# Performance work log

Measured on AMD Instinct MI355X. Metric: run time of the kernel, lower is better.

## Reference

```python
import jax, jax.numpy as jnp
import numpy as np

B, C, H, W = 8, 512, 32, 32
N_HEADS = 4
D_K = C // N_HEADS  # 128


def setup_inputs() -> dict:
    key = jax.random.key(0)
    k1, k2, k3, k4, k5 = jax.random.split(key, 5)
    x = jax.random.normal(k1, (B, C, H, W), dtype=jnp.float32)
    # projection: Linear(in_ch, n_heads*d_k*3)
    Wp = jax.random.normal(k2, (C, N_HEADS * D_K * 3), dtype=jnp.float32) * (C ** -0.5)
    bp = jax.random.normal(k3, (N_HEADS * D_K * 3,), dtype=jnp.float32) * 0.01
    # output: Linear(n_heads*d_k, in_ch)
    Wo = jax.random.normal(k4, (N_HEADS * D_K, C), dtype=jnp.float32) * ((N_HEADS * D_K) ** -0.5)
    bo = jax.random.normal(k5, (C,), dtype=jnp.float32) * 0.01
    return {"x": x, "Wp": Wp, "bp": bp, "Wo": Wo, "bo": bo}


def reference(x, Wp, bp, Wo, bo):
    b, c, h, w = x.shape
    scale = D_K ** -0.5
    # [B, C, H, W] -> [B, N, C], N = H*W
    xs = x.reshape(b, c, h * w).transpose(0, 2, 1)
    qkv = (xs @ Wp + bp).reshape(b, h * w, N_HEADS, 3 * D_K)
    q, k, v = jnp.split(qkv, 3, axis=-1)  # each [B, N, H, D]
    attn = jnp.einsum('bihd,bjhd->bijh', q, k) * scale
    attn = jax.nn.softmax(attn, axis=2)  # softmax over j (keys)
    out = jnp.einsum('bijh,bjhd->bihd', attn, v)
    out = out.reshape(b, h * w, N_HEADS * D_K)
    out = out @ Wo + bo
    out = out + xs  # residual (note: GroupNorm is unused in the original forward)
    return out.transpose(0, 2, 1).reshape(b, c, h, w)
```

## Files before the change

kernel.cpp:

```cpp
#include <hip/hip_runtime.h>

#define NB 8
#define NC 512
#define NTOK 1024
#define NHEADS 4
#define DKH 128

typedef unsigned short u16;
typedef __attribute__((ext_vector_type(8))) short bf16x8;
typedef __attribute__((ext_vector_type(4))) float f32x4;

__device__ inline u16 f2b(float f) {
    union { float f; unsigned u; } v; v.f = f;
    unsigned r = v.u + 0x7fffu + ((v.u >> 16) & 1u);
    return (u16)(r >> 16);
}

__device__ __forceinline__ void gll16(const u16* g, u16* l) {
    __builtin_amdgcn_global_load_lds((const __attribute__((address_space(1))) unsigned*)g,
                                     (__attribute__((address_space(3))) unsigned*)l, 16, 0, 0);
}

__global__ __launch_bounds__(256) void prep(const float* __restrict__ x, const float* __restrict__ Wp,
                                            const float* __restrict__ Wo,
                                            u16* __restrict__ xsb, u16* __restrict__ WpT, u16* __restrict__ WoT)
{
    __shared__ float tile[32][33];
    const int z = blockIdx.z;
    const float* src; u16* dst; int R, Cc;
    if (z == 0)      { src = Wp; dst = WpT; R = 512; Cc = 1536; }
    else if (z == 1) { if (blockIdx.x >= 16) return; src = Wo; dst = WoT; R = 512; Cc = 512; }
    else             { if (blockIdx.x >= 32) return;
                       src = x + (long)(z-2)*NC*NTOK; dst = xsb + (long)(z-2)*NTOK*NC; R = NC; Cc = NTOK; }
    int c0 = blockIdx.x * 32, r0 = blockIdx.y * 32;
    int tx = threadIdx.x, ty = threadIdx.y;
    #pragma unroll
    for (int k = 0; k < 4; ++k)
        tile[ty + 8*k][tx] = src[(long)(r0 + ty + 8*k) * Cc + c0 + tx];
    __syncthreads();
    #pragma unroll
    for (int k = 0; k < 4; ++k)
        dst[(long)(c0 + ty + 8*k) * R + r0 + tx] = f2b(tile[tx][ty + 8*k]);
}

__global__ __launch_bounds__(256) void gemm_qkv(const u16* __restrict__ WpT, const u16* __restrict__ xsb,
                                                const float* __restrict__ bp,
                                                u16* __restrict__ qg, u16* __restrict__ kg, u16* __restrict__ vg)
{
    __shared__ union SmU {
        struct { u16 As[128][64]; u16 Bs[128][64]; } s;
        u16 Os[4][64][72];
    } sm;
    const int tid = threadIdx.x;
    const int m0 = blockIdx.x * 128;
    const int n0 = blockIdx.y * 128;
    const int w = tid >> 6, lane = tid & 63, quad = lane >> 4, lc = lane & 15;
    const int mo = (w & 1) * 64, no = (w >> 1) * 64;
    const int sw8 = (((lane & 7) ^ (lane >> 3)) << 3);
    const int xs = lc & 7;

    f32x4 acc[4][4] = {};

    for (int k0 = 0; k0 < NC; k0 += 64) {
        __syncthreads();
        #pragma unroll
        for (int p = 0; p < 4; ++p) {
            int row = w*32 + p*8 + (lane >> 3);
            gll16(&WpT[(long)(m0 + row) * NC + k0 + sw8], &sm.s.As[w*32 + p*8][0]);
            gll16(&xsb[(long)(n0 + row) * NC + k0 + sw8], &sm.s.Bs[w*32 + p*8][0]);
        }
        __syncthreads();
        #pragma unroll
        for (int ks = 0; ks < 2; ++ks) {
            bf16x8 af[4], bfr[4];
            #pragma unroll
            for (int t = 0; t < 4; ++t) {
                af[t]  = *(const bf16x8*)&sm.s.As[mo + t*16 + lc][((ks*4 + quad) ^ xs) << 3];
                bfr[t] = *(const bf16x8*)&sm.s.Bs[no + t*16 + lc][((ks*4 + quad) ^ xs) << 3];
            }
            #pragma unroll
            for (int mt = 0; mt < 4; ++mt)
                #pragma unroll
                for (int nt = 0; nt < 4; ++nt)
                    acc[mt][nt] = __builtin_amdgcn_mfma_f32_16x16x32_bf16(af[mt], bfr[nt], acc[mt][nt], 0, 0, 0);
        }
    }
    __syncthreads();

    const int bb = n0 >> 10;
    const int nblk = n0 & 1023;
    const int cqb = m0 + mo;
    const int h = cqb / 384;
    const int rem = cqb - h * 384;
    const int sel = rem >> 7;
    const int d_base = rem & 127;

    #pragma unroll
    for (int mt = 0; mt < 4; ++mt) {
        int cq0 = cqb + mt*16 + quad*4;
        float b0 = bp[cq0+0], b1 = bp[cq0+1], b2 = bp[cq0+2], b3 = bp[cq0+3];
        #pragma unroll
        for (int nt = 0; nt < 4; ++nt) {
            f32x4 a = acc[mt][nt];
            int nl = nt*16 + lc;
            int ml = mt*16 + quad*4;
            u16 e0 = f2b(a[0]+b0), e1 = f2b(a[1]+b1), e2 = f2b(a[2]+b2), e3 = f2b(a[3]+b3);
            if (sel == 2) {
                sm.Os[w][ml+0][nl] = e0; sm.Os[w][ml+1][nl] = e1;
                sm.Os[w][ml+2][nl] = e2; sm.Os[w][ml+3][nl] = e3;
            } else {
                sm.Os[w][nl][ml+0] = e0; sm.Os[w][nl][ml+1] = e1;
                sm.Os[w][nl][ml+2] = e2; sm.Os[w][nl][ml+3] = e3;
            }
        }
    }
    __builtin_amdgcn_sched_barrier(0);

    const long bhbase = (long)(bb * NHEADS + h);
    const int sw = sw8;
    if (sel == 2) {
        #pragma unroll
        for (int pass = 0; pass < 8; ++pass) {
            int ml  = pass*8 + (lane >> 3);
            int nl0 = (lane & 7) * 8;
            bf16x8 vv = *(const bf16x8*)&sm.Os[w][ml][nl0];
            *(bf16x8*)&vg[((bhbase*DKH + d_base + ml) << 10) + nblk + no + sw] = vv;
        }
    } else if (sel == 1) {
        #pragma unroll
        for (int pass = 0; pass < 8; ++pass) {
            int nl  = pass*8 + (lane >> 3);
            int ml0 = (lane & 7) * 8;
            bf16x8 vv = *(const bf16x8*)&sm.Os[w][nl][ml0];
            *(bf16x8*)&kg[((bhbase*NTOK + nblk + no + nl) << 7) + d_base + sw] = vv;
        }
    } else {
        #pragma unroll
        for (int pass = 0; pass < 8; ++pass) {
            int nl  = pass*8 + (lane >> 3);
            int ml0 = (lane & 7) * 8;
            bf16x8 vv = *(const bf16x8*)&sm.Os[w][nl][ml0];
            *(bf16x8*)&qg[((bhbase*NTOK + nblk + no + nl) << 7) + d_base + ml0] = vv;
        }
    }
}

__global__ __launch_bounds__(256) void attn(const u16* __restrict__ qg, const u16* __restrict__ kg,
                                            const u16* __restrict__ vtg, u16* __restrict__ ho)
{
    __shared__ u16 Ks[2][64*128];
    __shared__ u16 Vt[2][128*64];
    __shared__ u16 Ps[4][32][72];
    const int tid = threadIdx.x;
    const int w = tid >> 6, lane = tid & 63, quad = lane >> 4, lc = lane & 15;
    const int id = blockIdx.x;
    const int xcd = id & 7, rest = id >> 3, sub = rest & 3, bx = rest >> 2;
    const int pr = xcd + sub*8;
    const int b = pr >> 2, h = pr & 3;
    const int i0 = bx*128 + w*32;
    const long bh = (long)(b * NHEADS + h) << 17;
    const u16* qb = qg + bh;
    const u16* kb = kg + bh;
    const u16* vb = vtg + bh;
    const float SL2E = 0.08838834764831845f * 1.4426950408889634f;

    bf16x8 qf[2][4];
    #pragma unroll
    for (int ib = 0; ib < 2; ++ib)
        #pragma unroll
        for (int ks = 0; ks < 4; ++ks)
            qf[ib][ks] = *(const bf16x8*)&qb[(long)(i0 + ib*16 + lc) * DKH + ks*32 + quad*8];

    f32x4 o[2][8] = {};
    float lsum[2] = {0.f, 0.f};
    const int xs = lc & 7;

    #pragma unroll
    for (int p = 0; p < 4; ++p) {
        int ck = (w*4 + p)*64 + lane;
        gll16(&kb[(long)ck * 8], &Ks[0][(w*4 + p)*512]);
        gll16(&vb[(((long)(ck >> 3)) << 10) + (ck & 7)*8], &Vt[0][(w*4 + p)*512]);
    }

    for (int t = 0; t < 16; ++t) {
        __syncthreads();
        if (t < 15) {
            long jo = (long)(t+1) * 64;
            #pragma unroll
            for (int p = 0; p < 4; ++p) {
                int ck = (w*4 + p)*64 + lane;
                gll16(&kb[jo*128 + (long)ck*8], &Ks[(t+1)&1][(w*4 + p)*512]);
                gll16(&vb[(((long)(ck >> 3)) << 10) + jo + (ck & 7)*8], &Vt[(t+1)&1][(w*4 + p)*512]);
            }
        }
        const u16* K = Ks[t&1];
        const u16* V = Vt[t&1];

        f32x4 s[2][4] = {};
        #pragma unroll
        for (int ks = 0; ks < 4; ++ks)
            #pragma unroll
            for (int jt = 0; jt < 4; ++jt) {
                bf16x8 kf = *(const bf16x8*)&K[(jt*16 + lc)*128 + (((ks*4 + quad) ^ xs) << 3)];
                s[0][jt] = __builtin_amdgcn_mfma_f32_16x16x32_bf16(kf, qf[0][ks], s[0][jt], 0, 0, 0);
                s[1][jt] = __builtin_amdgcn_mfma_f32_16x16x32_bf16(kf, qf[1][ks], s[1][jt], 0, 0, 0);
            }

        #pragma unroll
        for (int ib = 0; ib < 2; ++ib)
            #pragma unroll
            for (int jt = 0; jt < 4; ++jt) {
                float p0 = __builtin_amdgcn_exp2f(s[ib][jt][0] * SL2E);
                float p1 = __builtin_amdgcn_exp2f(s[ib][jt][1] * SL2E);
                float p2 = __builtin_amdgcn_exp2f(s[ib][jt][2] * SL2E);
                float p3 = __builtin_amdgcn_exp2f(s[ib][jt][3] * SL2E);
                lsum[ib] += (p0 + p1) + (p2 + p3);
                ushort4 pk;
                pk.x = f2b(p0); pk.y = f2b(p1); pk.z = f2b(p2); pk.w = f2b(p3);
                *(ushort4*)&Ps[w][ib*16 + lc][jt*16 + quad*4] = pk;
            }
        __builtin_amdgcn_sched_barrier(0);

        #pragma unroll
        for (int ks2 = 0; ks2 < 2; ++ks2) {
            bf16x8 pf0 = *(const bf16x8*)&Ps[w][lc][ks2*32 + quad*8];
            bf16x8 pf1 = *(const bf16x8*)&Ps[w][16 + lc][ks2*32 + quad*8];
            #pragma unroll
            for (int dt = 0; dt < 8; ++dt) {
                bf16x8 vf = *(const bf16x8*)&V[(dt*16 + lc)*64 + (((ks2*4 + quad) ^ xs) << 3)];
                o[0][dt] = __builtin_amdgcn_mfma_f32_16x16x32_bf16(vf, pf0, o[0][dt], 0, 0, 0);
                o[1][dt] = __builtin_amdgcn_mfma_f32_16x16x32_bf16(vf, pf1, o[1][dt], 0, 0, 0);
            }
        }
    }

    #pragma unroll
    for (int ib = 0; ib < 2; ++ib) {
        float l = lsum[ib];
        l += __shfl_xor(l, 16);
        l += __shfl_xor(l, 32);
        float inv = 1.0f / l;
        #pragma unroll
        for (int dt = 0; dt < 8; ++dt) {
            ushort4 pk;
            pk.x = f2b(o[ib][dt][0] * inv); pk.y = f2b(o[ib][dt][1] * inv);
            pk.z = f2b(o[ib][dt][2] * inv); pk.w = f2b(o[ib][dt][3] * inv);
            *(ushort4*)&ho[(long)(b*NTOK + i0 + ib*16 + lc) * NC + h*DKH + dt*16 + quad*4] = pk;
        }
    }
}

__global__ __launch_bounds__(256) void gemm_out(const u16* __restrict__ WoT, const u16* __restrict__ ho,
                                                const float* __restrict__ bo, const float* __restrict__ xin,
                                                float* __restrict__ dout)
{
    __shared__ struct { u16 As[128][64]; u16 Bs[64][64]; } sm;
    const int tid = threadIdx.x;
    const int m0 = blockIdx.x * 128;
    const int n0 = blockIdx.y * 64;
    const int w = tid >> 6, lane = tid & 63, quad = lane >> 4, lc = lane & 15;
    const int mo = (w & 1) * 64, no = (w >> 1) * 32;
    const int sw8 = (((lane & 7) ^ (lane >> 3)) << 3);
    const int xs = lc & 7;

    f32x4 acc[4][2] = {};

    for (int k0 = 0; k0 < NC; k0 += 64) {
        __syncthreads();
        #pragma unroll
        for (int p = 0; p < 4; ++p) {
            int row = w*32 + p*8 + (lane >> 3);
            gll16(&WoT[(long)(m0 + row) * NC + k0 + sw8], &sm.As[w*32 + p*8][0]);
        }
        #pragma unroll
        for (int p = 0; p < 2; ++p) {
            int row = w*16 + p*8 + (lane >> 3);
            gll16(&ho[(long)(n0 + row) * NC + k0 + sw8], &sm.Bs[w*16 + p*8][0]);
        }
        __syncthreads();
        #pragma unroll
        for (int ks = 0; ks < 2; ++ks) {
            bf16x8 af[4], bfr[2];
            #pragma unroll
            for (int t = 0; t < 4; ++t)
                af[t] = *(const bf16x8*)&sm.As[mo + t*16 + lc][((ks*4 + quad) ^ xs) << 3];
            #pragma unroll
            for (int t = 0; t < 2; ++t)
                bfr[t] = *(const bf16x8*)&sm.Bs[no + t*16 + lc][((ks*4 + quad) ^ xs) << 3];
            #pragma unroll
            for (int mt = 0; mt < 4; ++mt)
                #pragma unroll
                for (int nt = 0; nt < 2; ++nt)
                    acc[mt][nt] = __builtin_amdgcn_mfma_f32_16x16x32_bf16(af[mt], bfr[nt], acc[mt][nt], 0, 0, 0);
        }
    }

    const int bb = n0 >> 10;
    #pragma unroll
    for (int mt = 0; mt < 4; ++mt) {
        int cc0 = m0 + mo + mt*16 + quad*4;
        float b0 = bo[cc0+0], b1 = bo[cc0+1], b2 = bo[cc0+2], b3 = bo[cc0+3];
        #pragma unroll
        for (int nt = 0; nt < 2; ++nt) {
            int nl = (n0 + no + nt*16 + lc) & (NTOK - 1);
            f32x4 a = acc[mt][nt];
            long ix = ((long)(bb*NC + cc0) << 10) + nl;
            dout[ix]             = a[0] + b0 + xin[ix];
            dout[ix + (1 << 10)] = a[1] + b1 + xin[ix + (1 << 10)];
            dout[ix + (2 << 10)] = a[2] + b2 + xin[ix + (2 << 10)];
            dout[ix + (3 << 10)] = a[3] + b3 + xin[ix + (3 << 10)];
        }
    }
}

extern "C" void kernel_launch(void* const* d_in, const int* in_sizes, int n_in,
                              void* d_out, int out_size, void* d_ws, size_t ws_size,
                              hipStream_t stream)
{
    (void)in_sizes; (void)n_in; (void)out_size; (void)ws_size;
    const float* x  = (const float*)d_in[0];
    const float* Wp = (const float*)d_in[1];
    const float* bp = (const float*)d_in[2];
    const float* Wo = (const float*)d_in[3];
    const float* bo = (const float*)d_in[4];
    float* out = (float*)d_out;

    u16* ws  = (u16*)d_ws;
    u16* xsb = ws;
    u16* WpT = xsb + (long)NB * NTOK * NC;
    u16* WoT = WpT + 1536L * 512;
    u16* qg  = WoT + 512L * 512;
    u16* kg  = qg + (long)NB * NHEADS * NTOK * DKH;
    u16* vtg = kg + (long)NB * NHEADS * NTOK * DKH;
    u16* ho  = vtg + (long)NB * NHEADS * NTOK * DKH;

    prep<<<dim3(48, 16, 10), dim3(32, 8), 0, stream>>>(x, Wp, Wo, xsb, WpT, WoT);
    gemm_qkv<<<dim3(1536/128, (NB*NTOK)/128), 256, 0, stream>>>(WpT, xsb, bp, qg, kg, vtg);
    attn<<<dim3(256), 256, 0, stream>>>(qg, kg, vtg, ho);
    gemm_out<<<dim3(NC/128, (NB*NTOK)/64), 256, 0, stream>>>(WoT, ho, bo, x, out);
}
```

Baseline: 144.9 us.

## Split attention key tiles across two wave groups and merge partial outputs in LDS

The attention kernel now launches 512 threads per block, and two groups of four waves each process half of every 64-key tile for the same query rows. Each group keeps its own partial output accumulators and row sums, which are combined through a shared-memory buffer that reuses the K/V staging space at the end. This doubles the waves available per block to hide MFMA and exp latency with the same 256-block grid, at the cost of an extra LDS reduction pass and fewer K/V loads per wave. The launch-bounds hint may also change register allocation for the larger block.

```diff
diff --git a/kernel.cpp b/kernel.cpp
--- a/kernel.cpp
+++ b/kernel.cpp
@@ -145,19 +145,22 @@
     }
 }
 
-__global__ __launch_bounds__(256) void attn(const u16* __restrict__ qg, const u16* __restrict__ kg,
-                                            const u16* __restrict__ vtg, u16* __restrict__ ho)
-{
-    __shared__ u16 Ks[2][64*128];
-    __shared__ u16 Vt[2][128*64];
-    __shared__ u16 Ps[4][32][72];
+__global__ __launch_bounds__(512, 2) void attn(const u16* __restrict__ qg, const u16* __restrict__ kg,
+                                               const u16* __restrict__ vtg, u16* __restrict__ ho)
+{
+    __shared__ union {
+        struct { u16 Ks[2][64*128]; u16 Vt[2][128*64]; } kv;
+        struct { float Om[4][32][132]; float Ls[4][32]; } mg;
+    } sm;
+    __shared__ u16 Ps[8][32][40];
     const int tid = threadIdx.x;
     const int w = tid >> 6, lane = tid & 63, quad = lane >> 4, lc = lane & 15;
+    const int iw = w & 3, jh = w >> 2;
     const int id = blockIdx.x;
     const int xcd = id & 7, rest = id >> 3, sub = rest & 3, bx = rest >> 2;
     const int pr = xcd + sub*8;
     const int b = pr >> 2, h = pr & 3;
-    const int i0 = bx*128 + w*32;
+    const int i0 = bx*128 + iw*32;
     const long bh = (long)(b * NHEADS + h) << 17;
     const u16* qb = qg + bh;
     const u16* kb = kg + bh;
@@ -176,10 +179,10 @@
     const int xs = lc & 7;
 
     #pragma unroll
-    for (int p = 0; p < 4; ++p) {
-        int ck = (w*4 + p)*64 + lane;
-        gll16(&kb[(long)ck * 8], &Ks[0][(w*4 + p)*512]);
-        gll16(&vb[(((long)(ck >> 3)) << 10) + (ck & 7)*8], &Vt[0][(w*4 + p)*512]);
+    for (int p = 0; p < 2; ++p) {
+        int ck = (w*2 + p)*64 + lane;
+        gll16(&kb[(long)ck * 8], &sm.kv.Ks[0][(w*2 + p)*512]);
+        gll16(&vb[(((long)(ck >> 3)) << 10) + (ck & 7)*8], &sm.kv.Vt[0][(w*2 + p)*512]);
     }
 
     for (int t = 0; t < 16; ++t) {
@@ -187,21 +190,21 @@
         if (t < 15) {
             long jo = (long)(t+1) * 64;
             #pragma unroll
-            for (int p = 0; p < 4; ++p) {
-                int ck = (w*4 + p)*64 + lane;
-                gll16(&kb[jo*128 + (long)ck*8], &Ks[(t+1)&1][(w*4 + p)*512]);
-                gll16(&vb[(((long)(ck >> 3)) << 10) + jo + (ck & 7)*8], &Vt[(t+1)&1][(w*4 + p)*512]);
-            }
-        }
-        const u16* K = Ks[t&1];
-        const u16* V = Vt[t&1];
-
-        f32x4 s[2][4] = {};
+            for (int p = 0; p < 2; ++p) {
+                int ck = (w*2 + p)*64 + lane;
+                gll16(&kb[jo*128 + (long)ck*8], &sm.kv.Ks[(t+1)&1][(w*2 + p)*512]);
+                gll16(&vb[(((long)(ck >> 3)) << 10) + jo + (ck & 7)*8], &sm.kv.Vt[(t+1)&1][(w*2 + p)*512]);
+            }
+        }
+        const u16* K = sm.kv.Ks[t&1];
+        const u16* V = sm.kv.Vt[t&1];
+
+        f32x4 s[2][2] = {};
         #pragma unroll
         for (int ks = 0; ks < 4; ++ks)
             #pragma unroll
-            for (int jt = 0; jt < 4; ++jt) {
-                bf16x8 kf = *(const bf16x8*)&K[(jt*16 + lc)*128 + (((ks*4 + quad) ^ xs) << 3)];
+            for (int jt = 0; jt < 2; ++jt) {
+                bf16x8 kf = *(const bf16x8*)&K[(jh*32 + jt*16 + lc)*128 + (((ks*4 + quad) ^ xs) << 3)];
                 s[0][jt] = __builtin_amdgcn_mfma_f32_16x16x32_bf16(kf, qf[0][ks], s[0][jt], 0, 0, 0);
                 s[1][jt] = __builtin_amdgcn_mfma_f32_16x16x32_bf16(kf, qf[1][ks], s[1][jt], 0, 0, 0);
             }
@@ -209,7 +212,7 @@
         #pragma unroll
         for (int ib = 0; ib < 2; ++ib)
             #pragma unroll
-            for (int jt = 0; jt < 4; ++jt) {
+            for (int jt = 0; jt < 2; ++jt) {
                 float p0 = __builtin_amdgcn_exp2f(s[ib][jt][0] * SL2E);
                 float p1 = __builtin_amdgcn_exp2f(s[ib][jt][1] * SL2E);
                 float p2 = __builtin_amdgcn_exp2f(s[ib][jt][2] * SL2E);
@@ -221,13 +224,12 @@
             }
         __builtin_amdgcn_sched_barrier(0);
 
-        #pragma unroll
-        for (int ks2 = 0; ks2 < 2; ++ks2) {
-            bf16x8 pf0 = *(const bf16x8*)&Ps[w][lc][ks2*32 + quad*8];
-            bf16x8 pf1 = *(const bf16x8*)&Ps[w][16 + lc][ks2*32 + quad*8];
+        {
+            bf16x8 pf0 = *(const bf16x8*)&Ps[w][lc][quad*8];
+            bf16x8 pf1 = *(const bf16x8*)&Ps[w][16 + lc][quad*8];
             #pragma unroll
             for (int dt = 0; dt < 8; ++dt) {
-                bf16x8 vf = *(const bf16x8*)&V[(dt*16 + lc)*64 + (((ks2*4 + quad) ^ xs) << 3)];
+                bf16x8 vf = *(const bf16x8*)&V[(dt*16 + lc)*64 + (((jh*4 + quad) ^ xs) << 3)];
                 o[0][dt] = __builtin_amdgcn_mfma_f32_16x16x32_bf16(vf, pf0, o[0][dt], 0, 0, 0);
                 o[1][dt] = __builtin_amdgcn_mfma_f32_16x16x32_bf16(vf, pf1, o[1][dt], 0, 0, 0);
             }
@@ -236,16 +238,32 @@
 
     #pragma unroll
     for (int ib = 0; ib < 2; ++ib) {
-        float l = lsum[ib];
-        l += __shfl_xor(l, 16);
-        l += __shfl_xor(l, 32);
-        float inv = 1.0f / l;
-        #pragma unroll
-        for (int dt = 0; dt < 8; ++dt) {
-            ushort4 pk;
-            pk.x = f2b(o[ib][dt][0] * inv); pk.y = f2b(o[ib][dt][1] * inv);
-            pk.z = f2b(o[ib][dt][2] * inv); pk.w = f2b(o[ib][dt][3] * inv);
-            *(ushort4*)&ho[(long)(b*NTOK + i0 + ib*16 + lc) * NC + h*DKH + dt*16 + quad*4] = pk;
+        lsum[ib] += __shfl_xor(lsum[ib], 16);
+        lsum[ib] += __shfl_xor(lsum[ib], 32);
+    }
+
+    __syncthreads();
+    if (jh == 1) {
+        #pragma unroll
+        for (int ib = 0; ib < 2; ++ib)
+            #pragma unroll
+            for (int dt = 0; dt < 8; ++dt)
+                *(f32x4*)&sm.mg.Om[iw][ib*16 + lc][dt*16 + quad*4] = o[ib][dt];
+        if (quad == 0) { sm.mg.Ls[iw][lc] = lsum[0]; sm.mg.Ls[iw][16 + lc] = lsum[1]; }
+    }
+    __syncthreads();
+    if (jh == 0) {
+        #pragma unroll
+        for (int ib = 0; ib < 2; ++ib) {
+            float inv = 1.0f / (lsum[ib] + sm.mg.Ls[iw][ib*16 + lc]);
+            #pragma unroll
+            for (int dt = 0; dt < 8; ++dt) {
+                f32x4 oo = o[ib][dt] + *(const f32x4*)&sm.mg.Om[iw][ib*16 + lc][dt*16 + quad*4];
+                ushort4 pk;
+                pk.x = f2b(oo[0] * inv); pk.y = f2b(oo[1] * inv);
+                pk.z = f2b(oo[2] * inv); pk.w = f2b(oo[3] * inv);
+                *(ushort4*)&ho[(long)(b*NTOK + i0 + ib*16 + lc) * NC + h*DKH + dt*16 + quad*4] = pk;
+            }
         }
     }
 }
@@ -336,6 +354,6 @@
 
     prep<<<dim3(48, 16, 10), dim3(32, 8), 0, stream>>>(x, Wp, Wo, xsb, WpT, WoT);
     gemm_qkv<<<dim3(1536/128, (NB*NTOK)/128), 256, 0, stream>>>(WpT, xsb, bp, qg, kg, vtg);
-    attn<<<dim3(256), 256, 0, stream>>>(qg, kg, vtg, ho);
+    attn<<<dim3(256), 512, 0, stream>>>(qg, kg, vtg, ho);
     gemm_out<<<dim3(NC/128, (NB*NTOK)/64), 256, 0, stream>>>(WoT, ho, bo, x, out);
 }
```

Result: no change. 142.4 us (-1.7%).
